# Performance work log

Hardware: AMD Instinct MI355X
Metric: run time of the kernel (lower is better)

## Reference

```python
import jax, jax.numpy as jnp
import numpy as np

EPS = 1e-5

def setup_inputs() -> dict:
    key = jax.random.key(0)
    k1, k2, k3, k4, k5 = jax.random.split(key, 5)
    B, S, D, N = 4, 512, 768, 64
    return {
        "x": jax.random.uniform(k1, (B, S, D), dtype=jnp.float32),
        "A": jax.random.uniform(k2, (D, N), dtype=jnp.float32),
        "B_weight_raw": jax.random.normal(k3, (N, D), dtype=jnp.float32),
        "C_weight_raw": jax.random.normal(k4, (D, N), dtype=jnp.float32),
        "norm_gamma_raw": jax.random.normal(k5, (D,), dtype=jnp.float32),
    }

def reference(x, A, B_weight_raw, C_weight_raw, norm_gamma_raw):
    # x: [B, S, D]
    Bsz, S, D = x.shape
    N = A.shape[1]
    A_gate = jax.nn.sigmoid(A)                      # [D, N]
    Bw = jax.nn.sigmoid(B_weight_raw)               # [N, D] (TopologicalLinear: sigmoid-constrained weights)
    Cw = jax.nn.sigmoid(C_weight_raw)               # [D, N]
    gamma = jax.nn.sigmoid(norm_gamma_raw)          # [D]  (TopologicalNorm: layernorm w/ sigmoid scale)

    h0 = jnp.zeros((Bsz, D, N), dtype=x.dtype)

    def step(h, x_t):
        # x_t: [B, D]
        inp = x_t @ Bw.T                            # [B, N]
        morph = inp[:, None, :] * x_t[:, :, None]   # [B, D, N]
        h = jnp.clip(h * A_gate + morph, 0.0, 1.0)  # bounded state update
        y = jnp.sum(h * Cw, axis=-1)                # [B, D]
        mu = jnp.mean(y, axis=-1, keepdims=True)
        var = jnp.var(y, axis=-1, keepdims=True)
        y = (y - mu) * jax.lax.rsqrt(var + EPS) * gamma
        return h, y

    h_final, ys = jax.lax.scan(step, h0, jnp.swapaxes(x, 0, 1))  # ys: [S, B, D]
    y = jnp.swapaxes(ys, 0, 1)                                    # [B, S, D]
    return jnp.clip(y + x, 0.0, 1.0), h_final
```

## Files before the change

### kernel.cpp

```cpp
#include <hip/hip_runtime.h>
#include <math.h>

#define DD 768
#define NN 64
#define SS 512
#define BB 4
#define BSD (BB * SS * DD)

__device__ __forceinline__ float sigmf(float v) { return 1.0f / (1.0f + expf(-v)); }

template <int CTRL>
__device__ __forceinline__ float dppadd(float v) {
    int s = __builtin_amdgcn_update_dpp(0, __float_as_int(v), CTRL, 0xF, 0xF, true);
    return v + __int_as_float(s);
}
__device__ __forceinline__ float row_sum15(float v) {
    v = dppadd<0x111>(v);
    v = dppadd<0x112>(v);
    v = dppadd<0x114>(v);
    v = dppadd<0x118>(v);
    return v;
}
__device__ __forceinline__ float wave_sum63(float v) {
    v = row_sum15(v);
    v = dppadd<0x142>(v);
    v = dppadd<0x143>(v);
    return v;
}

__global__ __launch_bounds__(256) void prep_xpose_kernel(const float* __restrict__ Braw,
                                                         const float* __restrict__ graw,
                                                         const float* __restrict__ x,
                                                         float* __restrict__ BwT,
                                                         float* __restrict__ gamma_s,
                                                         float* __restrict__ xT) {
    __shared__ float tile[64][65];
    int tx = threadIdx.x & 63;
    int tq = threadIdx.x >> 6;
    if (blockIdx.x < 12) {
        int d0 = blockIdx.x * 64;
#pragma unroll
        for (int i = 0; i < 16; ++i) {
            int n = tq + i * 4;
            tile[n][tx] = sigmf(Braw[n * DD + d0 + tx]);
        }
        __syncthreads();
#pragma unroll
        for (int i = 0; i < 16; ++i) {
            int dl = tq + i * 4;
            BwT[(d0 + dl) * NN + tx] = tile[tx][dl];
        }
        int gi = blockIdx.x * 256 + threadIdx.x;
        if (gi < DD) gamma_s[gi] = sigmf(graw[gi]);
    } else {
        int bidx = blockIdx.x - 12;
        int b  = bidx / 96;
        int r  = bidx - b * 96;
        int t0 = (r / 12) * 64;
        int d0 = (r % 12) * 64;
#pragma unroll
        for (int i = 0; i < 16; ++i) {
            int t = tq + i * 4;
            tile[t][tx] = x[((size_t)b * SS + t0 + t) * DD + d0 + tx];
        }
        __syncthreads();
#pragma unroll
        for (int i = 0; i < 16; ++i) {
            int dl = tq + i * 4;
            xT[((size_t)b * DD + d0 + dl) * SS + t0 + tx] = tile[tx][dl];
        }
    }
}

__global__ __launch_bounds__(256, 2) void inp_kernel(const float* __restrict__ x,
                                                     const float* __restrict__ BwT,
                                                     float* __restrict__ inp) {
    int w    = threadIdx.x >> 6;
    int lane = threadIdx.x & 63;
    int g = lane >> 4;
    int q = lane & 15;
    int r = blockIdx.x * 4 + w;
    const float*  xr  = x + (size_t)r * DD;
    const float4* bwg = (const float4*)BwT;

    __shared__ float4 bwlds[2][1024];

#pragma unroll
    for (int k = 0; k < 4; ++k)
        bwlds[0][threadIdx.x + k * 256] = bwg[threadIdx.x + k * 256];
    __syncthreads();

    float4 acc = {0.f, 0.f, 0.f, 0.f};
    for (int c = 0; c < 12; ++c) {
        int cur = c & 1;
        float4 s0, s1, s2, s3;
        if (c < 11) {
            int base = (c + 1) * 1024 + threadIdx.x;
            s0 = bwg[base];
            s1 = bwg[base + 256];
            s2 = bwg[base + 512];
            s3 = bwg[base + 768];
        }
        int d0 = c * 64;
#pragma unroll
        for (int jj = 0; jj < 4; ++jj) {
            int dbase = jj * 16 + g;
            float x0 = xr[d0 + dbase + 0];
            float x1 = xr[d0 + dbase + 4];
            float x2 = xr[d0 + dbase + 8];
            float x3 = xr[d0 + dbase + 12];
            float4 w0 = bwlds[cur][(dbase + 0) * 16 + q];
            float4 w1 = bwlds[cur][(dbase + 4) * 16 + q];
            float4 w2 = bwlds[cur][(dbase + 8) * 16 + q];
            float4 w3 = bwlds[cur][(dbase + 12) * 16 + q];
#define IFMA(W, X)                       \
    acc.x = fmaf(X, W.x, acc.x);         \
    acc.y = fmaf(X, W.y, acc.y);         \
    acc.z = fmaf(X, W.z, acc.z);         \
    acc.w = fmaf(X, W.w, acc.w);
            IFMA(w0, x0) IFMA(w1, x1) IFMA(w2, x2) IFMA(w3, x3)
        }
        if (c < 11) {
            int nb = cur ^ 1;
            bwlds[nb][threadIdx.x]       = s0;
            bwlds[nb][threadIdx.x + 256] = s1;
            bwlds[nb][threadIdx.x + 512] = s2;
            bwlds[nb][threadIdx.x + 768] = s3;
        }
        __syncthreads();
    }

#pragma unroll
    for (int off = 16; off <= 32; off <<= 1) {
        acc.x += __shfl_xor(acc.x, off, 64);
        acc.y += __shfl_xor(acc.y, off, 64);
        acc.z += __shfl_xor(acc.z, off, 64);
        acc.w += __shfl_xor(acc.w, off, 64);
    }
    if (lane < 16) ((float4*)(inp + (size_t)r * NN))[q] = acc;
}

__global__ __launch_bounds__(256, 3) void scan_kernel(const float* __restrict__ xT,
                                                      const float* __restrict__ Araw,
                                                      const float* __restrict__ Craw,
                                                      const float* __restrict__ inp,
                                                      float* __restrict__ Y,
                                                      float* __restrict__ hfin) {
    int w    = threadIdx.x >> 6;
    int lane = threadIdx.x & 63;
    int gb = blockIdx.x;
    int b  = gb / 192;
    int dg = gb - b * 192;
    int d  = dg * 4 + w;

    float a = sigmf(Araw[(size_t)d * NN + lane]);
    float c = sigmf(Craw[(size_t)d * NN + lane]);

    const float*  ip_ptr = inp + (size_t)(b * SS) * NN + lane;
    const float4* xt4    = (const float4*)(xT + ((size_t)b * DD + d) * SS);
    float*        y_d    = Y + (size_t)(b * SS) * DD + d;

    __shared__ float lds[4][2][8][64];

    int s8 = lane >> 3;
    int j8 = lane & 7;

    float Ai[8], Bi[8], Ci[8], Di[8];
    float4 Ax0, Ax1, Bx0, Bx1, Cx0, Cx1, Dx0, Dx1;
    float h = 0.f;

#define SPREF(P, T0)                                                       \
    {                                                                      \
        int tt_ = ((T0) < SS) ? (T0) : 0;                                  \
        _Pragma("unroll")                                                  \
        for (int i_ = 0; i_ < 8; ++i_) P##i[i_] = ip_ptr[(tt_ + i_) * NN]; \
        P##x0 = xt4[(tt_ >> 2) + 0];                                       \
        P##x1 = xt4[(tt_ >> 2) + 1];                                       \
    }
#define SCHUNK(P, T0, SL)                                                        \
    {                                                                            \
        const float xs_[8] = {P##x0.x, P##x0.y, P##x0.z, P##x0.w,                \
                              P##x1.x, P##x1.y, P##x1.z, P##x1.w};               \
        _Pragma("unroll")                                                        \
        for (int i_ = 0; i_ < 8; ++i_) {                                         \
            h = __builtin_amdgcn_fmed3f(fmaf(h, a, P##i[i_] * xs_[i_]), 0.f, 1.f); \
            lds[w][SL][i_][lane] = h * c;                                        \
        }                                                                        \
        float4 v0_ = *(const float4*)&lds[w][SL][s8][j8 * 8];                    \
        float4 v1_ = *(const float4*)&lds[w][SL][s8][j8 * 8 + 4];                \
        float s_ = ((v0_.x + v0_.y) + (v0_.z + v0_.w)) +                         \
                   ((v1_.x + v1_.y) + (v1_.z + v1_.w));                          \
        s_ = dppadd<0x111>(s_);                                                  \
        s_ = dppadd<0x112>(s_);                                                  \
        s_ = dppadd<0x114>(s_);                                                  \
        if (j8 == 7) y_d[((T0) + s8) * DD] = s_;                                 \
    }

    SPREF(A, 0)
    SPREF(B, 8)
    SPREF(C, 16)
    SPREF(D, 24)

    for (int t0 = 0; t0 < SS; t0 += 32) {
        SCHUNK(A, t0, 0)      SPREF(A, t0 + 32)
        SCHUNK(B, t0 + 8, 1)  SPREF(B, t0 + 40)
        SCHUNK(C, t0 + 16, 0) SPREF(C, t0 + 48)
        SCHUNK(D, t0 + 24, 1) SPREF(D, t0 + 56)
    }
    hfin[((size_t)b * DD + d) * NN + lane] = h;
}

__global__ __launch_bounds__(256) void scan_fb_kernel(const float* __restrict__ x,
                                                      const float* __restrict__ Araw,
                                                      const float* __restrict__ Craw,
                                                      const float* __restrict__ inp,
                                                      float* __restrict__ Y,
                                                      float* __restrict__ hfin) {
    int wid  = (blockIdx.x * 256 + threadIdx.x) >> 6;
    int lane = threadIdx.x & 63;
    int b = wid / DD;
    int d = wid - b * DD;

    float a = sigmf(Araw[d * NN + lane]);
    float c = sigmf(Craw[d * NN + lane]);

    const float* ip_ptr = inp + (b * SS) * NN + lane;
    const float* x_ptr  = x   + (b * SS) * DD + d;
    float*       y_ptr  = Y   + (b * SS) * DD + d;

    float cip[8], cxv[8], nip[8], nxv[8];
#pragma unroll
    for (int i = 0; i < 8; ++i) {
        cip[i] = ip_ptr[i * NN];
        cxv[i] = x_ptr[i * DD];
    }
    float h = 0.f;
    for (int t0 = 0; t0 < SS; t0 += 8) {
        int tn = t0 + 8;
        if (tn >= SS) tn = SS - 8;
#pragma unroll
        for (int i = 0; i < 8; ++i) {
            nip[i] = ip_ptr[(tn + i) * NN];
            nxv[i] = x_ptr[(tn + i) * DD];
        }
#pragma unroll
        for (int i = 0; i < 8; ++i) {
            h = __builtin_amdgcn_fmed3f(fmaf(h, a, cip[i] * cxv[i]), 0.f, 1.f);
            float v = wave_sum63(h * c);
            if (lane == 63) y_ptr[(t0 + i) * DD] = v;
        }
#pragma unroll
        for (int i = 0; i < 8; ++i) { cip[i] = nip[i]; cxv[i] = nxv[i]; }
    }
    hfin[(size_t)wid * NN + lane] = h;
}

__global__ __launch_bounds__(256) void ln_kernel(const float* __restrict__ x,
                                                 const float* __restrict__ gamma_s,
                                                 float* __restrict__ out) {
    int wid  = (blockIdx.x * 256 + threadIdx.x) >> 6;
    int lane = threadIdx.x & 63;
    float*       yr = out + (size_t)wid * DD;
    const float* xr = x   + (size_t)wid * DD;

    float4 y0 = ((const float4*)yr)[lane * 3 + 0];
    float4 y1 = ((const float4*)yr)[lane * 3 + 1];
    float4 y2 = ((const float4*)yr)[lane * 3 + 2];

    float s = ((y0.x + y0.y) + (y0.z + y0.w)) + ((y1.x + y1.y) + (y1.z + y1.w)) +
              ((y2.x + y2.y) + (y2.z + y2.w));
#pragma unroll
    for (int off = 32; off; off >>= 1) s += __shfl_xor(s, off, 64);
    float mu = s * (1.f / 768.f);

    float q = 0.f;
#define QACC(v)                 \
    {                           \
        float d0_ = (v) - mu;   \
        q = fmaf(d0_, d0_, q);  \
    }
    QACC(y0.x) QACC(y0.y) QACC(y0.z) QACC(y0.w)
    QACC(y1.x) QACC(y1.y) QACC(y1.z) QACC(y1.w)
    QACC(y2.x) QACC(y2.y) QACC(y2.z) QACC(y2.w)
#pragma unroll
    for (int off = 32; off; off >>= 1) q += __shfl_xor(q, off, 64);
    float inv = rsqrtf(q * (1.f / 768.f) + 1e-5f);

    float4 g0 = ((const float4*)gamma_s)[lane * 3 + 0];
    float4 g1 = ((const float4*)gamma_s)[lane * 3 + 1];
    float4 g2 = ((const float4*)gamma_s)[lane * 3 + 2];
    float4 x0 = ((const float4*)xr)[lane * 3 + 0];
    float4 x1 = ((const float4*)xr)[lane * 3 + 1];
    float4 x2 = ((const float4*)xr)[lane * 3 + 2];

#define FIN(yv, gv, xv) __builtin_amdgcn_fmed3f(fmaf((yv - mu) * inv, gv, xv), 0.f, 1.f)
    float4 o0, o1, o2;
    o0.x = FIN(y0.x, g0.x, x0.x); o0.y = FIN(y0.y, g0.y, x0.y);
    o0.z = FIN(y0.z, g0.z, x0.z); o0.w = FIN(y0.w, g0.w, x0.w);
    o1.x = FIN(y1.x, g1.x, x1.x); o1.y = FIN(y1.y, g1.y, x1.y);
    o1.z = FIN(y1.z, g1.z, x1.z); o1.w = FIN(y1.w, g1.w, x1.w);
    o2.x = FIN(y2.x, g2.x, x2.x); o2.y = FIN(y2.y, g2.y, x2.y);
    o2.z = FIN(y2.z, g2.z, x2.z); o2.w = FIN(y2.w, g2.w, x2.w);

    ((float4*)yr)[lane * 3 + 0] = o0;
    ((float4*)yr)[lane * 3 + 1] = o1;
    ((float4*)yr)[lane * 3 + 2] = o2;
}

extern "C" void kernel_launch(void* const* d_in, const int* in_sizes, int n_in,
                              void* d_out, int out_size, void* d_ws, size_t ws_size,
                              hipStream_t stream) {
    const float* x    = (const float*)d_in[0];
    const float* Araw = (const float*)d_in[1];
    const float* Braw = (const float*)d_in[2];
    const float* Craw = (const float*)d_in[3];
    const float* graw = (const float*)d_in[4];

    float* out  = (float*)d_out;
    float* hfin = out + (size_t)BSD;

    float* ws      = (float*)d_ws;
    float* BwT     = ws;
    float* gamma_s = ws + DD * NN;
    float* inp     = ws + DD * NN + DD;
    float* xT      = ws + DD * NN + DD + BB * SS * NN;

    size_t need = (size_t)(DD * NN + DD + (size_t)BB * SS * NN + (size_t)BSD) * sizeof(float);

    if (ws_size >= need) {
        prep_xpose_kernel<<<12 + BB * (SS / 64) * (DD / 64), 256, 0, stream>>>(
            Braw, graw, x, BwT, gamma_s, xT);
        inp_kernel<<<(BB * SS) / 4, 256, 0, stream>>>(x, BwT, inp);
        scan_kernel<<<BB * (DD / 4), 256, 0, stream>>>(xT, Araw, Craw, inp, out, hfin);
    } else {
        prep_xpose_kernel<<<12, 256, 0, stream>>>(Braw, graw, x, BwT, gamma_s, xT);
        inp_kernel<<<(BB * SS) / 4, 256, 0, stream>>>(x, BwT, inp);
        scan_fb_kernel<<<(BB * DD * NN) / 256, 256, 0, stream>>>(x, Araw, Craw, inp, out, hfin);
    }
    ln_kernel<<<(BB * SS * NN) / 256, 256, 0, stream>>>(x, gamma_s, out);
}
```

Measured before the change: 60.38 us.

## Split scan over time halves and store inp in vector-friendly transposed layout

The scan grid is doubled. The second-half blocks first recompute the state over the first 256 steps without producing outputs, then emit outputs for steps 256 to 511. This doubles parallelism and raises the occupancy hint, at the cost of redundant recurrence work for the second half. The inp tensor is rewritten in a [b][t/8][n][8] layout so each lane loads its 8 timesteps with two float4 loads instead of eight strided scalar loads. The producer now does strided scalar stores, and the fallback path is updated to the new layout.

```diff
diff --git a/kernel.cpp b/kernel.cpp
--- a/kernel.cpp
+++ b/kernel.cpp
@@ -137,18 +137,27 @@
         acc.z += __shfl_xor(acc.z, off, 64);
         acc.w += __shfl_xor(acc.w, off, 64);
     }
-    if (lane < 16) ((float4*)(inp + (size_t)r * NN))[q] = acc;
-}
-
-__global__ __launch_bounds__(256, 3) void scan_kernel(const float* __restrict__ xT,
+    if (lane < 16) {
+        int bb = r >> 9;
+        int tt = r & 511;
+        float* dst = inp + ((size_t)bb * 64 + (tt >> 3)) * 512 + (tt & 7);
+        dst[(4 * q + 0) * 8] = acc.x;
+        dst[(4 * q + 1) * 8] = acc.y;
+        dst[(4 * q + 2) * 8] = acc.z;
+        dst[(4 * q + 3) * 8] = acc.w;
+    }
+}
+
+__global__ __launch_bounds__(256, 6) void scan_kernel(const float* __restrict__ xT,
                                                       const float* __restrict__ Araw,
                                                       const float* __restrict__ Craw,
-                                                      const float* __restrict__ inp,
+                                                      const float* __restrict__ inpT,
                                                       float* __restrict__ Y,
                                                       float* __restrict__ hfin) {
     int w    = threadIdx.x >> 6;
     int lane = threadIdx.x & 63;
-    int gb = blockIdx.x;
+    int half = blockIdx.x & 1;
+    int gb   = blockIdx.x >> 1;
     int b  = gb / 192;
     int dg = gb - b * 192;
     int d  = dg * 4 + w;
@@ -156,64 +165,82 @@
     float a = sigmf(Araw[(size_t)d * NN + lane]);
     float c = sigmf(Craw[(size_t)d * NN + lane]);
 
-    const float*  ip_ptr = inp + (size_t)(b * SS) * NN + lane;
-    const float4* xt4    = (const float4*)(xT + ((size_t)b * DD + d) * SS);
-    float*        y_d    = Y + (size_t)(b * SS) * DD + d;
+    const float*  ipT = inpT + (size_t)b * (SS / 8) * NN * 8;
+    const float4* xt4 = (const float4*)(xT + ((size_t)b * DD + d) * SS);
+    float*        y_d = Y + (size_t)(b * SS) * DD + d;
 
     __shared__ float lds[4][2][8][64];
 
     int s8 = lane >> 3;
     int j8 = lane & 7;
 
-    float Ai[8], Bi[8], Ci[8], Di[8];
-    float4 Ax0, Ax1, Bx0, Bx1, Cx0, Cx1, Dx0, Dx1;
+    float4 Aip0, Aip1, Axv0, Axv1;
+    float4 Bip0, Bip1, Bxv0, Bxv1;
     float h = 0.f;
 
-#define SPREF(P, T0)                                                       \
-    {                                                                      \
-        int tt_ = ((T0) < SS) ? (T0) : 0;                                  \
-        _Pragma("unroll")                                                  \
-        for (int i_ = 0; i_ < 8; ++i_) P##i[i_] = ip_ptr[(tt_ + i_) * NN]; \
-        P##x0 = xt4[(tt_ >> 2) + 0];                                       \
-        P##x1 = xt4[(tt_ >> 2) + 1];                                       \
-    }
-#define SCHUNK(P, T0, SL)                                                        \
-    {                                                                            \
-        const float xs_[8] = {P##x0.x, P##x0.y, P##x0.z, P##x0.w,                \
-                              P##x1.x, P##x1.y, P##x1.z, P##x1.w};               \
-        _Pragma("unroll")                                                        \
-        for (int i_ = 0; i_ < 8; ++i_) {                                         \
-            h = __builtin_amdgcn_fmed3f(fmaf(h, a, P##i[i_] * xs_[i_]), 0.f, 1.f); \
-            lds[w][SL][i_][lane] = h * c;                                        \
-        }                                                                        \
-        float4 v0_ = *(const float4*)&lds[w][SL][s8][j8 * 8];                    \
-        float4 v1_ = *(const float4*)&lds[w][SL][s8][j8 * 8 + 4];                \
-        float s_ = ((v0_.x + v0_.y) + (v0_.z + v0_.w)) +                         \
-                   ((v1_.x + v1_.y) + (v1_.z + v1_.w));                          \
-        s_ = dppadd<0x111>(s_);                                                  \
-        s_ = dppadd<0x112>(s_);                                                  \
-        s_ = dppadd<0x114>(s_);                                                  \
-        if (j8 == 7) y_d[((T0) + s8) * DD] = s_;                                 \
-    }
-
-    SPREF(A, 0)
-    SPREF(B, 8)
-    SPREF(C, 16)
-    SPREF(D, 24)
-
-    for (int t0 = 0; t0 < SS; t0 += 32) {
-        SCHUNK(A, t0, 0)      SPREF(A, t0 + 32)
-        SCHUNK(B, t0 + 8, 1)  SPREF(B, t0 + 40)
-        SCHUNK(C, t0 + 16, 0) SPREF(C, t0 + 48)
-        SCHUNK(D, t0 + 24, 1) SPREF(D, t0 + 56)
-    }
-    hfin[((size_t)b * DD + d) * NN + lane] = h;
+#define VPREF(P, T0)                                                              \
+    {                                                                             \
+        int tt_ = ((T0) < SS) ? (T0) : 0;                                         \
+        const float4* pp_ = (const float4*)(ipT + ((tt_ >> 3) * 64 + lane) * 8);  \
+        P##ip0 = pp_[0];                                                          \
+        P##ip1 = pp_[1];                                                          \
+        P##xv0 = xt4[(tt_ >> 2) + 0];                                             \
+        P##xv1 = xt4[(tt_ >> 2) + 1];                                             \
+    }
+#define VPRE(P)                                                                   \
+    {                                                                             \
+        const float xs_[8] = {P##xv0.x, P##xv0.y, P##xv0.z, P##xv0.w,             \
+                              P##xv1.x, P##xv1.y, P##xv1.z, P##xv1.w};            \
+        const float is_[8] = {P##ip0.x, P##ip0.y, P##ip0.z, P##ip0.w,             \
+                              P##ip1.x, P##ip1.y, P##ip1.z, P##ip1.w};            \
+        _Pragma("unroll")                                                         \
+        for (int i_ = 0; i_ < 8; ++i_)                                            \
+            h = __builtin_amdgcn_fmed3f(fmaf(h, a, is_[i_] * xs_[i_]), 0.f, 1.f); \
+    }
+#define VCHUNK(P, T0, SL)                                                         \
+    {                                                                             \
+        const float xs_[8] = {P##xv0.x, P##xv0.y, P##xv0.z, P##xv0.w,             \
+                              P##xv1.x, P##xv1.y, P##xv1.z, P##xv1.w};            \
+        const float is_[8] = {P##ip0.x, P##ip0.y, P##ip0.z, P##ip0.w,             \
+                              P##ip1.x, P##ip1.y, P##ip1.z, P##ip1.w};            \
+        _Pragma("unroll")                                                         \
+        for (int i_ = 0; i_ < 8; ++i_) {                                          \
+            h = __builtin_amdgcn_fmed3f(fmaf(h, a, is_[i_] * xs_[i_]), 0.f, 1.f); \
+            lds[w][SL][i_][lane] = h * c;                                         \
+        }                                                                         \
+        float4 v0_ = *(const float4*)&lds[w][SL][s8][j8 * 8];                     \
+        float4 v1_ = *(const float4*)&lds[w][SL][s8][j8 * 8 + 4];                 \
+        float s_ = ((v0_.x + v0_.y) + (v0_.z + v0_.w)) +                          \
+                   ((v1_.x + v1_.y) + (v1_.z + v1_.w));                           \
+        s_ = dppadd<0x111>(s_);                                                   \
+        s_ = dppadd<0x112>(s_);                                                   \
+        s_ = dppadd<0x114>(s_);                                                   \
+        if (j8 == 7) y_d[((T0) + s8) * DD] = s_;                                  \
+    }
+
+    if (half) {
+        VPREF(A, 0)
+        VPREF(B, 8)
+        for (int t0 = 0; t0 < 256; t0 += 16) {
+            VPRE(A) VPREF(A, t0 + 16)
+            VPRE(B) VPREF(B, t0 + 24)
+        }
+    }
+
+    int tb = half * 256;
+    VPREF(A, tb)
+    VPREF(B, tb + 8)
+    for (int t0 = tb; t0 < tb + 256; t0 += 16) {
+        VCHUNK(A, t0, 0)     VPREF(A, t0 + 16)
+        VCHUNK(B, t0 + 8, 1) VPREF(B, t0 + 24)
+    }
+    if (half) hfin[((size_t)b * DD + d) * NN + lane] = h;
 }
 
 __global__ __launch_bounds__(256) void scan_fb_kernel(const float* __restrict__ x,
                                                       const float* __restrict__ Araw,
                                                       const float* __restrict__ Craw,
-                                                      const float* __restrict__ inp,
+                                                      const float* __restrict__ inpT,
                                                       float* __restrict__ Y,
                                                       float* __restrict__ hfin) {
     int wid  = (blockIdx.x * 256 + threadIdx.x) >> 6;
@@ -224,14 +251,16 @@
     float a = sigmf(Araw[d * NN + lane]);
     float c = sigmf(Craw[d * NN + lane]);
 
-    const float* ip_ptr = inp + (b * SS) * NN + lane;
-    const float* x_ptr  = x   + (b * SS) * DD + d;
-    float*       y_ptr  = Y   + (b * SS) * DD + d;
+    const float* ipT   = inpT + (size_t)b * (SS / 8) * NN * 8;
+    const float* x_ptr = x + (b * SS) * DD + d;
+    float*       y_ptr = Y + (b * SS) * DD + d;
+
+#define IPAT(T) ipT[(((T) >> 3) * 64 + lane) * 8 + ((T) & 7)]
 
     float cip[8], cxv[8], nip[8], nxv[8];
 #pragma unroll
     for (int i = 0; i < 8; ++i) {
-        cip[i] = ip_ptr[i * NN];
+        cip[i] = IPAT(i);
         cxv[i] = x_ptr[i * DD];
     }
     float h = 0.f;
@@ -240,7 +269,7 @@
         if (tn >= SS) tn = SS - 8;
 #pragma unroll
         for (int i = 0; i < 8; ++i) {
-            nip[i] = ip_ptr[(tn + i) * NN];
+            nip[i] = IPAT(tn + i);
             nxv[i] = x_ptr[(tn + i) * DD];
         }
 #pragma unroll
@@ -331,7 +360,7 @@
         prep_xpose_kernel<<<12 + BB * (SS / 64) * (DD / 64), 256, 0, stream>>>(
             Braw, graw, x, BwT, gamma_s, xT);
         inp_kernel<<<(BB * SS) / 4, 256, 0, stream>>>(x, BwT, inp);
-        scan_kernel<<<BB * (DD / 4), 256, 0, stream>>>(xT, Araw, Craw, inp, out, hfin);
+        scan_kernel<<<BB * (DD / 4) * 2, 256, 0, stream>>>(xT, Araw, Craw, inp, out, hfin);
     } else {
         prep_xpose_kernel<<<12, 256, 0, stream>>>(Braw, graw, x, BwT, gamma_s, xT);
         inp_kernel<<<(BB * SS) / 4, 256, 0, stream>>>(x, BwT, inp);
```

New measurement: 82.34 us. 1.36x slower.

## Split scan time axis across two blocks with redundant h recompute

Applied to the files above, without the earlier changes.

Launches twice as many scan blocks. Each (b,d) group is split into two halves of the sequence: the second-half block first recomputes the recurrence over the first 256 steps without output (cheap FMA/clamp only), then produces outputs for steps 256-511 and writes the final state. This doubles the parallelism from 768 to 1536 blocks so more of the GPU is busy and the serial chain per block is shortened, at the cost of redundant recurrence work and more input reads. It also cuts the prefetch buffers from 4 to 2 to raise occupancy (launch bound 6) and pads the LDS rows to 68 floats to reduce bank conflicts.

```diff
diff --git a/kernel.cpp b/kernel.cpp
--- a/kernel.cpp
+++ b/kernel.cpp
@@ -140,7 +140,7 @@
     if (lane < 16) ((float4*)(inp + (size_t)r * NN))[q] = acc;
 }
 
-__global__ __launch_bounds__(256, 3) void scan_kernel(const float* __restrict__ xT,
+__global__ __launch_bounds__(256, 6) void scan_kernel(const float* __restrict__ xT,
                                                       const float* __restrict__ Araw,
                                                       const float* __restrict__ Craw,
                                                       const float* __restrict__ inp,
@@ -148,7 +148,8 @@
                                                       float* __restrict__ hfin) {
     int w    = threadIdx.x >> 6;
     int lane = threadIdx.x & 63;
-    int gb = blockIdx.x;
+    int half = blockIdx.x & 1;
+    int gb   = blockIdx.x >> 1;
     int b  = gb / 192;
     int dg = gb - b * 192;
     int d  = dg * 4 + w;
@@ -160,13 +161,13 @@
     const float4* xt4    = (const float4*)(xT + ((size_t)b * DD + d) * SS);
     float*        y_d    = Y + (size_t)(b * SS) * DD + d;
 
-    __shared__ float lds[4][2][8][64];
+    __shared__ float lds[4][2][8][68];
 
     int s8 = lane >> 3;
     int j8 = lane & 7;
 
-    float Ai[8], Bi[8], Ci[8], Di[8];
-    float4 Ax0, Ax1, Bx0, Bx1, Cx0, Cx1, Dx0, Dx1;
+    float Ai[8], Bi[8];
+    float4 Ax0, Ax1, Bx0, Bx1;
     float h = 0.f;
 
 #define SPREF(P, T0)                                                       \
@@ -177,37 +178,50 @@
         P##x0 = xt4[(tt_ >> 2) + 0];                                       \
         P##x1 = xt4[(tt_ >> 2) + 1];                                       \
     }
-#define SCHUNK(P, T0, SL)                                                        \
-    {                                                                            \
-        const float xs_[8] = {P##x0.x, P##x0.y, P##x0.z, P##x0.w,                \
-                              P##x1.x, P##x1.y, P##x1.z, P##x1.w};               \
-        _Pragma("unroll")                                                        \
-        for (int i_ = 0; i_ < 8; ++i_) {                                         \
+#define HCH(P)                                                                    \
+    {                                                                             \
+        const float xs_[8] = {P##x0.x, P##x0.y, P##x0.z, P##x0.w,                 \
+                              P##x1.x, P##x1.y, P##x1.z, P##x1.w};                \
+        _Pragma("unroll")                                                         \
+        for (int i_ = 0; i_ < 8; ++i_)                                            \
             h = __builtin_amdgcn_fmed3f(fmaf(h, a, P##i[i_] * xs_[i_]), 0.f, 1.f); \
-            lds[w][SL][i_][lane] = h * c;                                        \
-        }                                                                        \
-        float4 v0_ = *(const float4*)&lds[w][SL][s8][j8 * 8];                    \
-        float4 v1_ = *(const float4*)&lds[w][SL][s8][j8 * 8 + 4];                \
-        float s_ = ((v0_.x + v0_.y) + (v0_.z + v0_.w)) +                         \
-                   ((v1_.x + v1_.y) + (v1_.z + v1_.w));                          \
-        s_ = dppadd<0x111>(s_);                                                  \
-        s_ = dppadd<0x112>(s_);                                                  \
-        s_ = dppadd<0x114>(s_);                                                  \
-        if (j8 == 7) y_d[((T0) + s8) * DD] = s_;                                 \
-    }
-
-    SPREF(A, 0)
-    SPREF(B, 8)
-    SPREF(C, 16)
-    SPREF(D, 24)
-
-    for (int t0 = 0; t0 < SS; t0 += 32) {
-        SCHUNK(A, t0, 0)      SPREF(A, t0 + 32)
-        SCHUNK(B, t0 + 8, 1)  SPREF(B, t0 + 40)
-        SCHUNK(C, t0 + 16, 0) SPREF(C, t0 + 48)
-        SCHUNK(D, t0 + 24, 1) SPREF(D, t0 + 56)
-    }
-    hfin[((size_t)b * DD + d) * NN + lane] = h;
+    }
+#define SCHUNK(P, T0, SL)                                                         \
+    {                                                                             \
+        const float xs_[8] = {P##x0.x, P##x0.y, P##x0.z, P##x0.w,                 \
+                              P##x1.x, P##x1.y, P##x1.z, P##x1.w};                \
+        _Pragma("unroll")                                                         \
+        for (int i_ = 0; i_ < 8; ++i_) {                                          \
+            h = __builtin_amdgcn_fmed3f(fmaf(h, a, P##i[i_] * xs_[i_]), 0.f, 1.f); \
+            lds[w][SL][i_][lane] = h * c;                                         \
+        }                                                                         \
+        float4 v0_ = *(const float4*)&lds[w][SL][s8][j8 * 8];                     \
+        float4 v1_ = *(const float4*)&lds[w][SL][s8][j8 * 8 + 4];                 \
+        float s_ = ((v0_.x + v0_.y) + (v0_.z + v0_.w)) +                          \
+                   ((v1_.x + v1_.y) + (v1_.z + v1_.w));                           \
+        s_ = dppadd<0x111>(s_);                                                   \
+        s_ = dppadd<0x112>(s_);                                                   \
+        s_ = dppadd<0x114>(s_);                                                   \
+        if (j8 == 7) y_d[((T0) + s8) * DD] = s_;                                  \
+    }
+
+    if (half) {
+        SPREF(A, 0)
+        SPREF(B, 8)
+        for (int t0 = 0; t0 < 256; t0 += 16) {
+            HCH(A) SPREF(A, t0 + 16)
+            HCH(B) SPREF(B, t0 + 24)
+        }
+    }
+
+    int tb = half * 256;
+    SPREF(A, tb)
+    SPREF(B, tb + 8)
+    for (int t0 = tb; t0 < tb + 256; t0 += 16) {
+        SCHUNK(A, t0, 0)     SPREF(A, t0 + 16)
+        SCHUNK(B, t0 + 8, 1) SPREF(B, t0 + 24)
+    }
+    if (half) hfin[((size_t)b * DD + d) * NN + lane] = h;
 }
 
 __global__ __launch_bounds__(256) void scan_fb_kernel(const float* __restrict__ x,
@@ -331,7 +345,7 @@
         prep_xpose_kernel<<<12 + BB * (SS / 64) * (DD / 64), 256, 0, stream>>>(
             Braw, graw, x, BwT, gamma_s, xT);
         inp_kernel<<<(BB * SS) / 4, 256, 0, stream>>>(x, BwT, inp);
-        scan_kernel<<<BB * (DD / 4), 256, 0, stream>>>(xT, Araw, Craw, inp, out, hfin);
+        scan_kernel<<<BB * (DD / 4) * 2, 256, 0, stream>>>(xT, Araw, Craw, inp, out, hfin);
     } else {
         prep_xpose_kernel<<<12, 256, 0, stream>>>(Braw, graw, x, BwT, gamma_s, xT);
         inp_kernel<<<(BB * SS) / 4, 256, 0, stream>>>(x, BwT, inp);
```

New measurement: 81.80 us. 1.35x slower.

## Stage scan inputs through LDS via async global_load_lds with ring buffer

Applied to the files above, without the earlier changes.

The scan kernel now stages the per-batch inp chunks and the xT row into shared memory with async global-to-LDS loads, using a 4-slot ring buffer and explicit vmcnt waits. The reduction of each chunk is deferred by one iteration so it overlaps the next chunk's recurrence, and y values are buffered in LDS and written out at the end. The goal is to hide global-load latency on the serial recurrence and cut register pressure. It adds more LDS use per block (dropping the occupancy hint of 3) and relies on hand-written waitcnt ordering. The inp layout edit is only an index rewrite, since (tt>>3)*8 + (tt&7) equals tt.

```diff
diff --git a/kernel.cpp b/kernel.cpp
--- a/kernel.cpp
+++ b/kernel.cpp
@@ -27,6 +27,11 @@
     v = dppadd<0x143>(v);
     return v;
 }
+
+typedef const __attribute__((address_space(1))) void* gas_ptr;
+typedef __attribute__((address_space(3))) void* las_ptr;
+#define GLL16(SRC, DST) \
+    __builtin_amdgcn_global_load_lds((gas_ptr)(SRC), (las_ptr)(DST), 16, 0, 0)
 
 __global__ __launch_bounds__(256) void prep_xpose_kernel(const float* __restrict__ Braw,
                                                          const float* __restrict__ graw,
@@ -137,15 +142,20 @@
         acc.z += __shfl_xor(acc.z, off, 64);
         acc.w += __shfl_xor(acc.w, off, 64);
     }
-    if (lane < 16) ((float4*)(inp + (size_t)r * NN))[q] = acc;
-}
-
-__global__ __launch_bounds__(256, 3) void scan_kernel(const float* __restrict__ xT,
-                                                      const float* __restrict__ Araw,
-                                                      const float* __restrict__ Craw,
-                                                      const float* __restrict__ inp,
-                                                      float* __restrict__ Y,
-                                                      float* __restrict__ hfin) {
+    if (lane < 16) {
+        int bb = r >> 9;
+        int tt = r & 511;
+        float* dst = inp + (((size_t)bb * 64 + (tt >> 3)) * 8 + (tt & 7)) * 64;
+        ((float4*)dst)[q] = acc;
+    }
+}
+
+__global__ __launch_bounds__(256) void scan_kernel(const float* __restrict__ xT,
+                                                   const float* __restrict__ Araw,
+                                                   const float* __restrict__ Craw,
+                                                   const float* __restrict__ inpT,
+                                                   float* __restrict__ Y,
+                                                   float* __restrict__ hfin) {
     int w    = threadIdx.x >> 6;
     int lane = threadIdx.x & 63;
     int gb = blockIdx.x;
@@ -156,56 +166,78 @@
     float a = sigmf(Araw[(size_t)d * NN + lane]);
     float c = sigmf(Craw[(size_t)d * NN + lane]);
 
-    const float*  ip_ptr = inp + (size_t)(b * SS) * NN + lane;
-    const float4* xt4    = (const float4*)(xT + ((size_t)b * DD + d) * SS);
-    float*        y_d    = Y + (size_t)(b * SS) * DD + d;
-
-    __shared__ float lds[4][2][8][64];
+    const float* ipb   = inpT + (size_t)b * 64 * 512;
+    const float* xtrow = xT + ((size_t)b * DD + d) * SS;
+    float*       y_d   = Y + (size_t)(b * SS) * DD + d;
+
+    __shared__ float ip[4][4][8][64];
+    __shared__ float xts[4][512];
+    __shared__ float ylds[4][512];
 
     int s8 = lane >> 3;
     int j8 = lane & 7;
 
-    float Ai[8], Bi[8], Ci[8], Di[8];
-    float4 Ax0, Ax1, Bx0, Bx1, Cx0, Cx1, Dx0, Dx1;
+    GLL16(xtrow + lane * 4,       &xts[w][0]);
+    GLL16(xtrow + 256 + lane * 4, &xts[w][256]);
+#pragma unroll
+    for (int k = 0; k < 3; ++k) {
+        GLL16(ipb + k * 512 + lane * 4,       &ip[w][k][0][0]);
+        GLL16(ipb + k * 512 + 256 + lane * 4, &ip[w][k][4][0]);
+    }
+
     float h = 0.f;
 
-#define SPREF(P, T0)                                                       \
-    {                                                                      \
-        int tt_ = ((T0) < SS) ? (T0) : 0;                                  \
-        _Pragma("unroll")                                                  \
-        for (int i_ = 0; i_ < 8; ++i_) P##i[i_] = ip_ptr[(tt_ + i_) * NN]; \
-        P##x0 = xt4[(tt_ >> 2) + 0];                                       \
-        P##x1 = xt4[(tt_ >> 2) + 1];                                       \
-    }
-#define SCHUNK(P, T0, SL)                                                        \
+#define CONSUME(CC, CS)                                                          \
     {                                                                            \
-        const float xs_[8] = {P##x0.x, P##x0.y, P##x0.z, P##x0.w,                \
-                              P##x1.x, P##x1.y, P##x1.z, P##x1.w};               \
+        float ipv_[8];                                                           \
+        _Pragma("unroll")                                                        \
+        for (int i_ = 0; i_ < 8; ++i_) ipv_[i_] = ip[w][CS][i_][lane];           \
+        float4 xv0_ = *(const float4*)&xts[w][(CC) * 8];                         \
+        float4 xv1_ = *(const float4*)&xts[w][(CC) * 8 + 4];                     \
+        const float xs_[8] = {xv0_.x, xv0_.y, xv0_.z, xv0_.w,                    \
+                              xv1_.x, xv1_.y, xv1_.z, xv1_.w};                   \
         _Pragma("unroll")                                                        \
         for (int i_ = 0; i_ < 8; ++i_) {                                         \
-            h = __builtin_amdgcn_fmed3f(fmaf(h, a, P##i[i_] * xs_[i_]), 0.f, 1.f); \
-            lds[w][SL][i_][lane] = h * c;                                        \
+            h = __builtin_amdgcn_fmed3f(fmaf(h, a, ipv_[i_] * xs_[i_]), 0.f, 1.f); \
+            ip[w][CS][i_][lane] = h * c;    \
         }                                                                        \
-        float4 v0_ = *(const float4*)&lds[w][SL][s8][j8 * 8];                    \
-        float4 v1_ = *(const float4*)&lds[w][SL][s8][j8 * 8 + 4];                \
+    }
+#define REDUCE(XX, PS)                                                           \
+    {                                                                            \
+        float4 v0_ = *(const float4*)&ip[w][PS][s8][j8 * 8];                     \
+        float4 v1_ = *(const float4*)&ip[w][PS][s8][j8 * 8 + 4];                 \
         float s_ = ((v0_.x + v0_.y) + (v0_.z + v0_.w)) +                         \
                    ((v1_.x + v1_.y) + (v1_.z + v1_.w));                          \
         s_ = dppadd<0x111>(s_);                                                  \
         s_ = dppadd<0x112>(s_);                                                  \
         s_ = dppadd<0x114>(s_);                                                  \
-        if (j8 == 7) y_d[((T0) + s8) * DD] = s_;                                 \
-    }
-
-    SPREF(A, 0)
-    SPREF(B, 8)
-    SPREF(C, 16)
-    SPREF(D, 24)
-
-    for (int t0 = 0; t0 < SS; t0 += 32) {
-        SCHUNK(A, t0, 0)      SPREF(A, t0 + 32)
-        SCHUNK(B, t0 + 8, 1)  SPREF(B, t0 + 40)
-        SCHUNK(C, t0 + 16, 0) SPREF(C, t0 + 48)
-        SCHUNK(D, t0 + 24, 1) SPREF(D, t0 + 56)
+        if (j8 == 7) ylds[w][(XX) * 8 + s8] = s_;                                \
+    }
+#define VWAIT                                           \
+    asm volatile("s_waitcnt vmcnt(4)" ::: "memory");    \
+    __builtin_amdgcn_sched_barrier(0);
+
+    {
+        GLL16(ipb + 2 * 512 + lane * 4,       &ip[w][2][0][0]);
+        GLL16(ipb + 2 * 512 + 256 + lane * 4, &ip[w][2][4][0]);
+        VWAIT
+        CONSUME(0, 0)
+    }
+    for (int cc = 1; cc < 64; ++cc) {
+        int ch = cc + 2; if (ch > 63) ch = 63;
+        int sl = (cc + 2) & 3;
+        GLL16(ipb + ch * 512 + lane * 4,       &ip[w][sl][0][0]);
+        GLL16(ipb + ch * 512 + 256 + lane * 4, &ip[w][sl][4][0]);
+        VWAIT
+        int cs = cc & 3;
+        CONSUME(cc, cs)
+        REDUCE(cc - 1, (cc - 1) & 3)
+    }
+    REDUCE(63, 3)
+#pragma unroll
+    for (int k = 0; k < 8; ++k) {
+        float v = ylds[w][lane + k * 64];
+        y_d[(size_t)(lane + k * 64) * DD] = v;
     }
     hfin[((size_t)b * DD + d) * NN + lane] = h;
 }
@@ -213,7 +245,7 @@
 __global__ __launch_bounds__(256) void scan_fb_kernel(const float* __restrict__ x,
                                                       const float* __restrict__ Araw,
                                                       const float* __restrict__ Craw,
-                                                      const float* __restrict__ inp,
+                                                      const float* __restrict__ inpT,
                                                       float* __restrict__ Y,
                                                       float* __restrict__ hfin) {
     int wid  = (blockIdx.x * 256 + threadIdx.x) >> 6;
@@ -224,14 +256,16 @@
     float a = sigmf(Araw[d * NN + lane]);
     float c = sigmf(Craw[d * NN + lane]);
 
-    const float* ip_ptr = inp + (b * SS) * NN + lane;
-    const float* x_ptr  = x   + (b * SS) * DD + d;
-    float*       y_ptr  = Y   + (b * SS) * DD + d;
+    const float* ipb   = inpT + (size_t)b * 64 * 512;
+    const float* x_ptr = x + (b * SS) * DD + d;
+    float*       y_ptr = Y + (b * SS) * DD + d;
+
+#define IPAT(T) ipb[(((T) >> 3) * 8 + ((T) & 7)) * 64 + lane]
 
     float cip[8], cxv[8], nip[8], nxv[8];
 #pragma unroll
     for (int i = 0; i < 8; ++i) {
-        cip[i] = ip_ptr[i * NN];
+        cip[i] = IPAT(i);
         cxv[i] = x_ptr[i * DD];
     }
     float h = 0.f;
@@ -240,7 +274,7 @@
         if (tn >= SS) tn = SS - 8;
 #pragma unroll
         for (int i = 0; i < 8; ++i) {
-            nip[i] = ip_ptr[(tn + i) * NN];
+            nip[i] = IPAT(tn + i);
             nxv[i] = x_ptr[(tn + i) * DD];
         }
 #pragma unroll
```

Measured after the change: 76.67 us. 27.0% more time.
